# Performance work log

Measured on AMD Instinct MI355X. Metric: run time of the kernel, lower is better.

The kernel has to match this reference:

```python
import jax, jax.numpy as jnp
import numpy as np

# torch semantics: m = x > 0; y = x[m]  (flattened stream compaction);
# unsqueeze(0) then squeeze([0]) is an identity.
# JAX/jit cannot return data-dependent shapes, so we return the compacted
# values moved to the front of a fixed-size buffer (padded with 0) plus the
# valid count. y_padded[:count] == torch's y.

def reference(x):
    xf = x.reshape(-1)                      # [N]
    mask = xf > 0.0                         # [N] bool
    count = jnp.sum(mask)                   # scalar int: number of valid elems
    # stable argsort on ~mask moves True-mask positions to the front,
    # preserving original order (matches masked_select ordering)
    order = jnp.argsort(jnp.logical_not(mask), stable=True)  # [N]
    n = xf.shape[0]
    y_padded = jnp.where(jnp.arange(n) < count, xf[order], 0.0)  # [N]
    return y_padded, count


def setup_inputs() -> dict:
    key = jax.random.key(0)
    x = jax.random.normal(key, (64, 1024, 1024), dtype=jnp.float32)
    return {"x": x}
```

## Files before the change

kernel.cpp:

```cpp
#include <hip/hip_runtime.h>


#define BLOCK 256
#define VPT 16
#define CHUNK (BLOCK * VPT)
#define SCAN_THREADS 1024
#define SCAN_VPT 16

__global__ void k_count(const float* __restrict__ x, int n, int* __restrict__ blockSums) {
    const int tid = threadIdx.x;
    const long long tbase = (long long)blockIdx.x * CHUNK + tid * VPT;
    int cnt = 0;
    if (tbase + VPT <= n) {
#pragma unroll
        for (int k = 0; k < 4; ++k) {
            const float4 v = *reinterpret_cast<const float4*>(x + tbase + 4 * k);
            cnt += (v.x > 0.f) + (v.y > 0.f) + (v.z > 0.f) + (v.w > 0.f);
        }
    } else {
        for (long long j = tbase; j < tbase + VPT && j < n; ++j) cnt += (x[j] > 0.f);
    }
#pragma unroll
    for (int off = 32; off > 0; off >>= 1) cnt += __shfl_down(cnt, off, 64);
    __shared__ int lds[4];
    if ((tid & 63) == 0) lds[tid >> 6] = cnt;
    __syncthreads();
    if (tid == 0) blockSums[blockIdx.x] = lds[0] + lds[1] + lds[2] + lds[3];
}

__global__ void k_scan(int* __restrict__ sums, int numBlocks,
                       int* __restrict__ countOut, float* __restrict__ countOutF) {
    __shared__ int lds[32];
    const int tid  = threadIdx.x;
    const int lane = tid & 63;
    const int wave = tid >> 6;

    int vals[SCAN_VPT];
    const int base = tid * SCAN_VPT;
    int local = 0;
#pragma unroll
    for (int j = 0; j < SCAN_VPT; ++j) {
        const int i = base + j;
        const int v = (i < numBlocks) ? sums[i] : 0;
        vals[j] = local;
        local += v;
    }
    int incl = local;
#pragma unroll
    for (int off = 1; off < 64; off <<= 1) {
        const int y = __shfl_up(incl, off, 64);
        if (lane >= off) incl += y;
    }
    if (lane == 63) lds[wave] = incl;
    __syncthreads();
    if (wave == 0 && lane < 16) {
        int w = lds[lane];
#pragma unroll
        for (int off = 1; off < 16; off <<= 1) {
            const int y = __shfl_up(w, off, 16);
            if ((lane & 15) >= off) w += y;
        }
        lds[16 + lane] = w;
    }
    __syncthreads();
    const int waveEx   = (wave == 0) ? 0 : lds[16 + wave - 1];
    const int threadEx = waveEx + incl - local;
#pragma unroll
    for (int j = 0; j < SCAN_VPT; ++j) {
        const int i = base + j;
        if (i < numBlocks) sums[i] = threadEx + vals[j];
    }
    if (tid == SCAN_THREADS - 1) {
        const int total = waveEx + incl;
        *countOut  = total;
        *countOutF = (float)total;
    }
}

__device__ __forceinline__ int block_scan_excl_256(int val, int* lds, int* blockTotal) {
    const int tid  = threadIdx.x;
    const int lane = tid & 63;
    const int wave = tid >> 6;
    int incl = val;
#pragma unroll
    for (int off = 1; off < 64; off <<= 1) {
        const int y = __shfl_up(incl, off, 64);
        if (lane >= off) incl += y;
    }
    if (lane == 63) lds[wave] = incl;
    __syncthreads();
    if (tid == 0) {
        const int s0 = lds[0], s1 = lds[1], s2 = lds[2], s3 = lds[3];
        lds[4] = 0; lds[5] = s0; lds[6] = s0 + s1; lds[7] = s0 + s1 + s2;
        lds[8] = s0 + s1 + s2 + s3;
    }
    __syncthreads();
    const int ex = lds[4 + wave] + incl - val;
    *blockTotal = lds[8];
    return ex;
}

__global__ void k_scatter(const float* __restrict__ x, int n,
                          const int* __restrict__ blockOffsets, float* __restrict__ y) {
    __shared__ float vals[CHUNK];
    __shared__ int scan_lds[9];
    const int tid = threadIdx.x;
    const long long tbase = (long long)blockIdx.x * CHUNK + tid * VPT;

    float v[VPT];
    if (tbase + VPT <= n) {
#pragma unroll
        for (int k = 0; k < 4; ++k) {
            const float4 f = *reinterpret_cast<const float4*>(x + tbase + 4 * k);
            v[4 * k + 0] = f.x; v[4 * k + 1] = f.y; v[4 * k + 2] = f.z; v[4 * k + 3] = f.w;
        }
    } else {
#pragma unroll
        for (int j = 0; j < VPT; ++j)
            v[j] = (tbase + j < n) ? x[tbase + j] : 0.f;
    }

    int c = 0;
#pragma unroll
    for (int j = 0; j < VPT; ++j) c += (v[j] > 0.f);

    int total;
    int r = block_scan_excl_256(c, scan_lds, &total);

#pragma unroll
    for (int j = 0; j < VPT; ++j) {
        if (v[j] > 0.f) vals[r++] = v[j];
    }
    __syncthreads();

    const int offset = blockOffsets[blockIdx.x];
    for (int j = tid; j < total; j += BLOCK) {
        y[offset + j] = vals[j];
    }
}

__global__ void k_zerofill(float* __restrict__ y, const int* __restrict__ count, int n) {
    const long long i = ((long long)blockIdx.x * BLOCK + threadIdx.x) * 4;
    if (i >= n) return;
    const int c = *count;
    if (i + 4 <= c) return;
    const long long start = (i > c) ? i : c;
    const long long end   = (i + 4 < n) ? i + 4 : n;
    if (start == i && end == i + 4) {
        *reinterpret_cast<float4*>(y + i) = make_float4(0.f, 0.f, 0.f, 0.f);
    } else {
        for (long long j = start; j < end; ++j) y[j] = 0.f;
    }
}

extern "C" void kernel_launch(void* const* d_in, const int* in_sizes, int n_in,
                              void* d_out, int out_size, void* d_ws, size_t ws_size,
                              hipStream_t stream) {
    const float* x = (const float*)d_in[0];
    float* y = (float*)d_out;
    const int n = in_sizes[0];

    int* blockSums = (int*)d_ws;
    const int numBlocks = (n + CHUNK - 1) / CHUNK;
    int* countPtr = blockSums + numBlocks;

    k_count<<<numBlocks, BLOCK, 0, stream>>>(x, n, blockSums);
    k_scan<<<1, SCAN_THREADS, 0, stream>>>(blockSums, numBlocks,
                                           countPtr, y + (out_size - 1));
    k_scatter<<<numBlocks, BLOCK, 0, stream>>>(x, n, blockSums, y);
    const int zfBlocks = ((n + 3) / 4 + BLOCK - 1) / BLOCK;
    k_zerofill<<<zfBlocks, BLOCK, 0, stream>>>(y, countPtr, n);
}
```

Before: 505.6 us.

## Fuse zero-fill into scatter kernel and coalesce count loads

Removes the separate zero-fill kernel. Each scatter block now writes its own share of zeros at the tail, computed from its exclusive offset, so the zero region is partitioned across blocks. The count kernel switches from per-thread contiguous float4 loads to block-strided coalesced float4 loads, and both kernels gain launch bounds. This saves one kernel launch and a full pass over the zero-filled tail of the output, at the cost of scattered tail writes from each block.

After: 493.7 us. -2.4%, faster.

```diff
diff --git a/kernel.cpp b/kernel.cpp
--- a/kernel.cpp
+++ b/kernel.cpp
@@ -7,18 +7,21 @@
 #define SCAN_THREADS 1024
 #define SCAN_VPT 16
 
-__global__ void k_count(const float* __restrict__ x, int n, int* __restrict__ blockSums) {
+__global__ void __launch_bounds__(BLOCK)
+k_count(const float* __restrict__ x, int n, int* __restrict__ blockSums) {
     const int tid = threadIdx.x;
-    const long long tbase = (long long)blockIdx.x * CHUNK + tid * VPT;
+    const long long chunkBase = (long long)blockIdx.x * CHUNK;
     int cnt = 0;
-    if (tbase + VPT <= n) {
+    if (chunkBase + CHUNK <= n) {
+        const float* p = x + chunkBase + tid * 4;
 #pragma unroll
-        for (int k = 0; k < 4; ++k) {
-            const float4 v = *reinterpret_cast<const float4*>(x + tbase + 4 * k);
+        for (int it = 0; it < 4; ++it) {
+            const float4 v = *reinterpret_cast<const float4*>(p + it * (BLOCK * 4));
             cnt += (v.x > 0.f) + (v.y > 0.f) + (v.z > 0.f) + (v.w > 0.f);
         }
     } else {
-        for (long long j = tbase; j < tbase + VPT && j < n; ++j) cnt += (x[j] > 0.f);
+        const long long lim = (chunkBase + CHUNK < n) ? chunkBase + CHUNK : n;
+        for (long long j = chunkBase + tid; j < lim; j += BLOCK) cnt += (x[j] > 0.f);
     }
 #pragma unroll
     for (int off = 32; off > 0; off >>= 1) cnt += __shfl_down(cnt, off, 64);
@@ -100,15 +103,17 @@
     return ex;
 }
 
-__global__ void k_scatter(const float* __restrict__ x, int n,
-                          const int* __restrict__ blockOffsets, float* __restrict__ y) {
+__global__ void __launch_bounds__(BLOCK)
+k_scatter(const float* __restrict__ x, int n,
+          const int* __restrict__ blockOffsets, float* __restrict__ y) {
     __shared__ float vals[CHUNK];
     __shared__ int scan_lds[9];
     const int tid = threadIdx.x;
-    const long long tbase = (long long)blockIdx.x * CHUNK + tid * VPT;
+    const int chunkBase = blockIdx.x * CHUNK;
+    const long long tbase = (long long)chunkBase + tid * VPT;
 
     float v[VPT];
-    if (tbase + VPT <= n) {
+    if ((long long)chunkBase + CHUNK <= n) {
 #pragma unroll
         for (int k = 0; k < 4; ++k) {
             const float4 f = *reinterpret_cast<const float4*>(x + tbase + 4 * k);
@@ -133,23 +138,19 @@
     }
     __syncthreads();
 
-    const int offset = blockOffsets[blockIdx.x];
+    const int excl = blockOffsets[blockIdx.x];
+
     for (int j = tid; j < total; j += BLOCK) {
-        y[offset + j] = vals[j];
+        y[excl + j] = vals[j];
     }
-}
 
-__global__ void k_zerofill(float* __restrict__ y, const int* __restrict__ count, int n) {
-    const long long i = ((long long)blockIdx.x * BLOCK + threadIdx.x) * 4;
-    if (i >= n) return;
-    const int c = *count;
-    if (i + 4 <= c) return;
-    const long long start = (i > c) ? i : c;
-    const long long end   = (i + 4 < n) ? i + 4 : n;
-    if (start == i && end == i + 4) {
-        *reinterpret_cast<float4*>(y + i) = make_float4(0.f, 0.f, 0.f, 0.f);
-    } else {
-        for (long long j = start; j < end; ++j) y[j] = 0.f;
+    const int rem   = n - chunkBase;
+    const int elems = rem < CHUNK ? rem : CHUNK;
+    const int z     = elems - total;
+    const long long zhi = (long long)n - (chunkBase - excl);
+    const long long zlo = zhi - z;
+    for (int j = tid; j < z; j += BLOCK) {
+        y[zlo + j] = 0.f;
     }
 }
 
@@ -168,6 +169,4 @@
     k_scan<<<1, SCAN_THREADS, 0, stream>>>(blockSums, numBlocks,
                                            countPtr, y + (out_size - 1));
     k_scatter<<<numBlocks, BLOCK, 0, stream>>>(x, n, blockSums, y);
-    const int zfBlocks = ((n + 3) / 4 + BLOCK - 1) / BLOCK;
-    k_zerofill<<<zfBlocks, BLOCK, 0, stream>>>(y, countPtr, n);
 }
```
